# Optimization experiments

Measured on AMD Instinct MI355X. Metric: run time of the kernel, lower is better.

## Reference

```python
import jax, jax.numpy as jnp
import numpy as np

# ---- static geometry (matches init_kwargs) ----
B, S, D = 2, 4096, 2048
H, HD = 32, 64                      # num_heads, head_dim
HGRID, WGRID = 64, 64               # canvas h_dim, w_dim
TH, TW = 8, 16                      # tile size (th*tw = 128)
KH, KW = 16, 32                     # window (kernel) size
NTH, NTW = HGRID // TH, WGRID // TW
T = NTH * NTW                       # 32 tiles
TN = TH * TW                        # 128 tokens per tile
KTH, KTW = KH // TH, KW // TW
K = KTH * KTW                       # 4 kv tiles per query tile
SCALE = 1.0 / np.sqrt(HD)


def _kv_tile_ids():
    # For each query tile, the K kv tiles inside its (clamped) sliding window.
    qt = np.arange(T)
    qh, qw = qt // NTW, qt % NTW
    lbh, rbh = KTH // 2, KTH // 2 + (KTH % 2 - 1)
    lbw, rbw = KTW // 2, KTW // 2 + (KTW % 2 - 1)
    ch = np.clip(qh, lbh, NTH - 1 - rbh)
    cw = np.clip(qw, lbw, NTW - 1 - rbw)
    hh = ch[:, None] - lbh + np.arange(KTH)          # [T, KTH]
    ww = cw[:, None] - lbw + np.arange(KTW)          # [T, KTW]
    return (hh[:, :, None] * NTW + ww[:, None, :]).reshape(T, K)

KV_TILES = jnp.asarray(_kv_tile_ids())  # [T, K] int


def _to_tiles(x):
    # [B, S, H, HD] (row-major h,w) -> [B, H, T, TN, HD] (tile-major)
    x = x.reshape(B, NTH, TH, NTW, TW, H, HD)
    x = x.transpose(0, 5, 1, 3, 2, 4, 6)  # B,H,nth,ntw,th,tw,hd
    return x.reshape(B, H, T, TN, HD)


def _from_tiles(x):
    # [B, H, T, TN, HD] -> [B, S, H*HD]
    x = x.reshape(B, H, NTH, NTW, TH, TW, HD)
    x = x.transpose(0, 2, 4, 3, 5, 1, 6)  # B,nth,th,ntw,tw,H,hd
    return x.reshape(B, S, H * HD)


def setup_inputs() -> dict:
    key = jax.random.key(0)
    ks = jax.random.split(key, 5)
    sw = 1.0 / np.sqrt(D)
    return {
        "hidden_states": jax.random.normal(ks[0], (B, S, D), jnp.float32),
        "Wq": jax.random.normal(ks[1], (D, D), jnp.float32) * sw,
        "Wk": jax.random.normal(ks[2], (D, D), jnp.float32) * sw,
        "Wv": jax.random.normal(ks[3], (D, D), jnp.float32) * sw,
        "Wo": jax.random.normal(ks[4], (D, D), jnp.float32) * sw,
    }


def reference(hidden_states, Wq, Wk, Wv, Wo):
    # projections (weights stored [in, out]; equivalent to nn.Linear math)
    q = _to_tiles((hidden_states @ Wq).reshape(B, S, H, HD))  # [B,H,T,TN,HD]
    k = _to_tiles((hidden_states @ Wk).reshape(B, S, H, HD))
    v = _to_tiles((hidden_states @ Wv).reshape(B, S, H, HD))

    # gather the K allowed kv tiles for every query tile (block-sparse pattern)
    kg = k[:, :, KV_TILES].reshape(B, H, T, K * TN, HD)  # [B,H,T,K*TN,HD]
    vg = v[:, :, KV_TILES].reshape(B, H, T, K * TN, HD)

    # dense attention within each block (all gathered tokens are valid)
    scores = jnp.einsum("bhtqd,bhtkd->bhtqk", q, kg) * SCALE
    attn = jax.nn.softmax(scores, axis=-1)
    o = jnp.einsum("bhtqk,bhtkd->bhtqd", attn, vg)  # [B,H,T,TN,HD]

    return _from_tiles(o) @ Wo  # [B, S, D]
```

## Files before the change

### kernel.cpp

```cpp
#include <hip/hip_runtime.h>

typedef __bf16 bf16;
typedef __attribute__((ext_vector_type(8))) __bf16 bf16x8;
typedef __attribute__((ext_vector_type(4))) __bf16 bf16x4;
typedef __attribute__((ext_vector_type(4))) float f32x4;

#define MFMA16(a, b, c) __builtin_amdgcn_mfma_f32_16x16x32_bf16((a), (b), (c), 0, 0, 0)

__device__ __forceinline__ void gload16(const void* g, void* lds) {
  __builtin_amdgcn_global_load_lds(
      (__attribute__((address_space(1))) unsigned int*)(unsigned long long)g,
      (__attribute__((address_space(3))) unsigned int*)lds, 16, 0, 0);
}

__global__ void __launch_bounds__(256) cast_x_kernel(const float* __restrict__ X,
                                                     bf16* __restrict__ Xb) {
  int i = (blockIdx.x * 256 + threadIdx.x) * 4;
  f32x4 v = *(const f32x4*)(X + i);
  bf16x4 o;
  o[0] = (bf16)v[0]; o[1] = (bf16)v[1]; o[2] = (bf16)v[2]; o[3] = (bf16)v[3];
  *(bf16x4*)(Xb + i) = o;
}

__global__ void __launch_bounds__(256) transpose_w3_kernel(const float* __restrict__ Wq,
                                                           const float* __restrict__ Wk,
                                                           const float* __restrict__ Wv,
                                                           bf16* __restrict__ T0,
                                                           bf16* __restrict__ T1,
                                                           bf16* __restrict__ T2) {
  __shared__ float tile[64][65];
  int which = blockIdx.x >> 10;
  int bid = blockIdx.x & 1023;
  const float* W = which == 0 ? Wq : (which == 1 ? Wk : Wv);
  bf16* WT = which == 0 ? T0 : (which == 1 ? T1 : T2);
  int n0 = (bid & 31) * 64;
  int k0 = (bid >> 5) * 64;
  int tid = threadIdx.x;
  int r = tid >> 4;
  int c4 = (tid & 15) * 4;
#pragma unroll
  for (int i = 0; i < 4; ++i) {
    f32x4 v = *(const f32x4*)(W + (size_t)(k0 + r + i * 16) * 2048 + n0 + c4);
    tile[r + i * 16][c4 + 0] = v[0];
    tile[r + i * 16][c4 + 1] = v[1];
    tile[r + i * 16][c4 + 2] = v[2];
    tile[r + i * 16][c4 + 3] = v[3];
  }
  __syncthreads();
#pragma unroll
  for (int i = 0; i < 4; ++i) {
    int n = r + i * 16;
    bf16x4 o;
    o[0] = (bf16)tile[c4 + 0][n];
    o[1] = (bf16)tile[c4 + 1][n];
    o[2] = (bf16)tile[c4 + 2][n];
    o[3] = (bf16)tile[c4 + 3][n];
    *(bf16x4*)(WT + (size_t)(n0 + n) * 2048 + k0 + c4) = o;
  }
}

__global__ void __launch_bounds__(256) transpose_w_kernel(const float* __restrict__ W,
                                                          bf16* __restrict__ WT) {
  __shared__ float tile[64][65];
  int n0 = (blockIdx.x & 31) * 64;
  int k0 = (blockIdx.x >> 5) * 64;
  int tid = threadIdx.x;
  int r = tid >> 4;
  int c4 = (tid & 15) * 4;
#pragma unroll
  for (int i = 0; i < 4; ++i) {
    f32x4 v = *(const f32x4*)(W + (size_t)(k0 + r + i * 16) * 2048 + n0 + c4);
    tile[r + i * 16][c4 + 0] = v[0];
    tile[r + i * 16][c4 + 1] = v[1];
    tile[r + i * 16][c4 + 2] = v[2];
    tile[r + i * 16][c4 + 3] = v[3];
  }
  __syncthreads();
#pragma unroll
  for (int i = 0; i < 4; ++i) {
    int n = r + i * 16;
    bf16x4 o;
    o[0] = (bf16)tile[c4 + 0][n];
    o[1] = (bf16)tile[c4 + 1][n];
    o[2] = (bf16)tile[c4 + 2][n];
    o[3] = (bf16)tile[c4 + 3][n];
    *(bf16x4*)(WT + (size_t)(n0 + n) * 2048 + k0 + c4) = o;
  }
}

__device__ __forceinline__ void gemm256_core(const bf16* __restrict__ Ag,
                                             const bf16* __restrict__ Bg,
                                             char* lds, f32x4 (&acc)[8][4]) {
  const int tid = threadIdx.x;
  const int lane = tid & 63, wid = tid >> 6;
  const int g = lane >> 4, r16 = lane & 15;
  const int wm = wid >> 2, wn = wid & 3;
  const int swz = ((g ^ ((r16 >> 1) & 3)) << 4);

  const int srow = wid * 32 + (lane >> 2);
  const int scol = ((lane & 3) ^ ((lane >> 3) & 3)) * 8;
  const bf16* gA = Ag + (size_t)srow * 2048 + scol;
  const bf16* gB = Bg + (size_t)srow * 2048 + scol;
  char* sA = lds + wid * 2048;
  char* sB = lds + 16384 + wid * 2048;

  const int arow0 = wm * 128 + r16;
  const int brow0 = wn * 64 + r16;

#define STAGE_A(bf_, tt_)                              \
  {                                                    \
    char* d_ = sA + (bf_) * 32768;                     \
    const bf16* s_ = gA + (size_t)(tt_) * 32;          \
    gload16(s_, d_);                                   \
    gload16(s_ + (size_t)16 * 2048, d_ + 1024);        \
  }
#define STAGE_B(bf_, tt_)                              \
  {                                                    \
    char* d_ = sB + (bf_) * 32768;                     \
    const bf16* s_ = gB + (size_t)(tt_) * 32;          \
    gload16(s_, d_);                                   \
    gload16(s_ + (size_t)16 * 2048, d_ + 1024);        \
  }

  STAGE_A(0, 0) STAGE_B(0, 0) STAGE_A(1, 1) STAGE_B(1, 1)
  asm volatile("s_waitcnt vmcnt(4)" ::: "memory");
  __builtin_amdgcn_s_barrier();
  __builtin_amdgcn_sched_barrier(0);

  int c = 0;
  for (int t = 0; t < 64; ++t) {
    const char* Ab = lds + c * 32768;
    const char* Bb = Ab + 16384;
    int sbuf = c + 2; if (sbuf >= 3) sbuf -= 3;

    bf16x8 bfr[4], af[8];
#pragma unroll
    for (int j = 0; j < 4; ++j)
      bfr[j] = *(const bf16x8*)(Bb + (brow0 + j * 16) * 64 + swz);
#pragma unroll
    for (int i = 0; i < 8; ++i)
      af[i] = *(const bf16x8*)(Ab + (arow0 + i * 16) * 64 + swz);

    if (t < 62) { STAGE_A(sbuf, t + 2) STAGE_B(sbuf, t + 2) }

#pragma unroll
    for (int i = 0; i < 8; ++i)
#pragma unroll
      for (int j = 0; j < 4; ++j)
        acc[i][j] = MFMA16(af[i], bfr[j], acc[i][j]);

    if (t < 62) {
      asm volatile("s_waitcnt vmcnt(4)" ::: "memory");
    } else if (t == 62) {
      asm volatile("s_waitcnt vmcnt(0)" ::: "memory");
    }
    __builtin_amdgcn_s_barrier();
    __builtin_amdgcn_sched_barrier(0);

    c += 1; if (c >= 3) c -= 3;
  }
#undef STAGE_A
#undef STAGE_B
}

__global__ void __launch_bounds__(512, 2) gemm_qkv_kernel(
    const bf16* __restrict__ Xb, const bf16* __restrict__ W0, const bf16* __restrict__ W1,
    const bf16* __restrict__ W2, bf16* __restrict__ q_t, bf16* __restrict__ k_t,
    bf16* __restrict__ v_t) {
  __shared__ char lds[98304];
  int bid = blockIdx.x;
  int xcd = bid & 7, idx = bid >> 3;
  int by = xcd * 4 + idx / 24, bx = idx % 24;
  int which = bx >> 3;
  int m0 = by * 256, n0 = (bx & 7) * 256;
  const bf16* W = which == 0 ? W0 : (which == 1 ? W1 : W2);

  f32x4 acc[8][4] = {};
  gemm256_core(Xb + (size_t)m0 * 2048, W + (size_t)n0 * 2048, lds, acc);

  int lane = threadIdx.x & 63, wid = threadIdx.x >> 6;
  int g = lane >> 4, r16 = lane & 15;
  int wm = wid >> 2, wn = wid & 3;
#pragma unroll
  for (int i = 0; i < 8; ++i) {
#pragma unroll
    for (int r = 0; r < 4; ++r) {
      int m = m0 + wm * 128 + i * 16 + g * 4 + r;
      int b = m >> 12, s = m & 4095;
      int hg = s >> 6, wg = s & 63;
      int t = ((hg >> 3) << 2) + (wg >> 4);
      int tn = ((hg & 7) << 4) + (wg & 15);
#pragma unroll
      for (int j = 0; j < 4; ++j) {
        int n = n0 + wn * 64 + j * 16 + r16;
        int h = n >> 6, hd = n & 63;
        float val = acc[i][j][r];
        size_t base = ((size_t)(b * 32 + h) * 32 + t);
        if (which == 0)
          q_t[(base * 128 + tn) * 64 + hd] = (bf16)(val * 0.18033688056680255f);
        else if (which == 1)
          k_t[(base * 128 + tn) * 64 + hd] = (bf16)val;
        else
          v_t[(base * 64 + hd) * 128 + tn] = (bf16)val;
      }
    }
  }
}

__global__ void __launch_bounds__(512, 2) gemm_out_kernel(const bf16* __restrict__ A,
                                                          const bf16* __restrict__ W,
                                                          float* __restrict__ C) {
  __shared__ char lds[98304];
  int bid = blockIdx.x;
  int xcd = bid & 7, idx = bid >> 3;
  int by = xcd * 4 + idx / 8, bx = idx & 7;
  int m0 = by * 256, n0 = bx * 256;

  f32x4 acc[8][4] = {};
  gemm256_core(A + (size_t)m0 * 2048, W + (size_t)n0 * 2048, lds, acc);

  int lane = threadIdx.x & 63, wid = threadIdx.x >> 6;
  int g = lane >> 4, r16 = lane & 15;
  int wm = wid >> 2, wn = wid & 3;
#pragma unroll
  for (int i = 0; i < 8; ++i)
#pragma unroll
    for (int j = 0; j < 4; ++j)
#pragma unroll
      for (int r = 0; r < 4; ++r) {
        int m = m0 + wm * 128 + i * 16 + g * 4 + r;
        int n = n0 + wn * 64 + j * 16 + r16;
        C[(size_t)m * 2048 + n] = acc[i][j][r];
      }
}

__global__ void __launch_bounds__(256) attn_kernel(const bf16* __restrict__ q_t,
                                                   const bf16* __restrict__ k_t,
                                                   const bf16* __restrict__ v_t,
                                                   bf16* __restrict__ o_bf) {
  __shared__ char Pl[128 * 256];
  int bid = blockIdx.x;
  int bh = (bid & 7) * 8 + (bid >> 8);
  int t = (bid >> 3) & 31;
  int h = bh & 31, b = bh >> 5;
  int tid = threadIdx.x, w = tid >> 6, lane = tid & 63;
  int g = lane >> 4, r16 = lane & 15;

  const size_t qoff = ((size_t)bh * 32 + t) * (128 * 64);
  bf16x8 qf[2][2];
#pragma unroll
  for (int mf = 0; mf < 2; ++mf)
#pragma unroll
    for (int kf = 0; kf < 2; ++kf)
      qf[mf][kf] = *(const bf16x8*)&q_t[qoff + (size_t)(w * 32 + mf * 16 + r16) * 64 + kf * 32 + g * 8];

  bf16x8 ones;
#pragma unroll
  for (int j = 0; j < 8; ++j) ones[j] = (bf16)1.0f;

  f32x4 oacc[2][4] = {};
  f32x4 lacc[2] = {};

  int qh = t >> 2, qw = t & 3;
  int ch = qh < 1 ? 1 : (qh > 7 ? 7 : qh);
  int cw = qw < 1 ? 1 : (qw > 3 ? 3 : qw);

  for (int c = 0; c < 4; ++c) {
    int vt = (ch - 1 + (c >> 1)) * 4 + (cw - 1 + (c & 1));
    const bf16* Kt = k_t + ((size_t)bh * 32 + vt) * (128 * 64);
    const bf16* Vt = v_t + ((size_t)bh * 32 + vt) * (128 * 64);

    f32x4 s[2][8];
#pragma unroll
    for (int nf = 0; nf < 8; ++nf) {
      bf16x8 kf0 = *(const bf16x8*)&Kt[(nf * 16 + r16) * 64 + g * 8];
      bf16x8 kf1 = *(const bf16x8*)&Kt[(nf * 16 + r16) * 64 + 32 + g * 8];
#pragma unroll
      for (int mf = 0; mf < 2; ++mf) {
        f32x4 z = {};
        z = MFMA16(qf[mf][0], kf0, z);
        z = MFMA16(qf[mf][1], kf1, z);
        s[mf][nf] = z;
      }
    }

#pragma unroll
    for (int mf = 0; mf < 2; ++mf)
#pragma unroll
      for (int r = 0; r < 4; ++r) {
        int row = w * 32 + mf * 16 + g * 4 + r;
        int rb = row * 256;
        int swzp = (row & 7) << 4;
#pragma unroll
        for (int nf = 0; nf < 8; ++nf) {
          int addr = (rb + (nf * 16 + r16) * 2) ^ swzp;
          *(bf16*)(Pl + addr) = (bf16)__builtin_amdgcn_exp2f(s[mf][nf][r]);
        }
      }
    __syncthreads();

#pragma unroll
    for (int ks = 0; ks < 4; ++ks) {
      bf16x8 pf[2];
#pragma unroll
      for (int mf = 0; mf < 2; ++mf) {
        int row = w * 32 + mf * 16 + r16;
        int addr = (row * 256 + ks * 64 + g * 16) ^ ((row & 7) << 4);
        pf[mf] = *(const bf16x8*)(Pl + addr);
      }
      bf16x8 vf[4];
#pragma unroll
      for (int hf = 0; hf < 4; ++hf)
        vf[hf] = *(const bf16x8*)&Vt[(hf * 16 + r16) * 128 + ks * 32 + g * 8];
#pragma unroll
      for (int mf = 0; mf < 2; ++mf) {
        lacc[mf] = MFMA16(pf[mf], ones, lacc[mf]);
#pragma unroll
        for (int hf = 0; hf < 4; ++hf)
          oacc[mf][hf] = MFMA16(pf[mf], vf[hf], oacc[mf][hf]);
      }
    }
    __syncthreads();
  }

  int nth = t >> 2, ntw = t & 3;
#pragma unroll
  for (int mf = 0; mf < 2; ++mf)
#pragma unroll
    for (int r = 0; r < 4; ++r) {
      float inv = __builtin_amdgcn_rcpf(lacc[mf][r]);
      int tn = w * 32 + mf * 16 + g * 4 + r;
      int stok = (nth * 8 + (tn >> 4)) * 64 + ntw * 16 + (tn & 15);
#pragma unroll
      for (int hf = 0; hf < 4; ++hf) {
        int col = h * 64 + hf * 16 + r16;
        o_bf[((size_t)b * 4096 + stok) * 2048 + col] = (bf16)(oacc[mf][hf][r] * inv);
      }
    }
}

extern "C" void kernel_launch(void* const* d_in, const int* in_sizes, int n_in,
                              void* d_out, int out_size, void* d_ws, size_t ws_size,
                              hipStream_t stream) {
  const float* X = (const float*)d_in[0];
  const float* Wq = (const float*)d_in[1];
  const float* Wk = (const float*)d_in[2];
  const float* Wv = (const float*)d_in[3];
  const float* Wo = (const float*)d_in[4];
  float* out = (float*)d_out;
  char* ws = (char*)d_ws;
  if (ws_size < 159383552u) return;

  bf16* Xb  = (bf16*)(ws + 0);
  bf16* WT0 = (bf16*)(ws + 33554432u);
  bf16* WT1 = (bf16*)(ws + 41943040u);
  bf16* WT2 = (bf16*)(ws + 50331648u);
  bf16* q_t = (bf16*)(ws + 58720256u);
  bf16* k_t = (bf16*)(ws + 92274688u);
  bf16* v_t = (bf16*)(ws + 125829120u);
  bf16* o_bf = Xb;

  cast_x_kernel<<<16384, 256, 0, stream>>>(X, Xb);
  transpose_w3_kernel<<<3072, 256, 0, stream>>>(Wq, Wk, Wv, WT0, WT1, WT2);
  gemm_qkv_kernel<<<768, 512, 0, stream>>>(Xb, WT0, WT1, WT2, q_t, k_t, v_t);
  attn_kernel<<<2048, 256, 0, stream>>>(q_t, k_t, v_t, o_bf);
  transpose_w_kernel<<<1024, 256, 0, stream>>>(Wo, WT0);
  gemm_out_kernel<<<256, 512, 0, stream>>>(o_bf, WT0, out);
}
```

Measured before the change: 458.0 us.

## Deepen GEMM LDS pipeline to four stages with register double-buffered fragments

The shared 256x256 GEMM core moves from a 3-buffer LDS ring to a 4-buffer ring, with loads issued three tiles ahead. The loop is unrolled by two with ping-pong register fragment sets, so the LDS reads for the next k-step are issued before the MFMAs of the current step. The aim is to hide global-load and LDS-read latency behind matrix math. In exchange, LDS per block grows to 128 KB, which likely allows only one block per CU despite the launch bound of two. The second fragment set also raises register pressure.

Measured after the change: 455.9 us. About the same (-0.5%).

```diff
diff --git a/kernel.cpp b/kernel.cpp
--- a/kernel.cpp
+++ b/kernel.cpp
@@ -107,67 +107,73 @@
   const int arow0 = wm * 128 + r16;
   const int brow0 = wn * 64 + r16;
 
-#define STAGE_A(bf_, tt_)                              \
-  {                                                    \
-    char* d_ = sA + (bf_) * 32768;                     \
-    const bf16* s_ = gA + (size_t)(tt_) * 32;          \
-    gload16(s_, d_);                                   \
-    gload16(s_ + (size_t)16 * 2048, d_ + 1024);        \
-  }
-#define STAGE_B(bf_, tt_)                              \
-  {                                                    \
-    char* d_ = sB + (bf_) * 32768;                     \
-    const bf16* s_ = gB + (size_t)(tt_) * 32;          \
-    gload16(s_, d_);                                   \
-    gload16(s_ + (size_t)16 * 2048, d_ + 1024);        \
-  }
-
-  STAGE_A(0, 0) STAGE_B(0, 0) STAGE_A(1, 1) STAGE_B(1, 1)
+#define STAGE(bf_, tt_)                                                  \
+  {                                                                      \
+    char* dA_ = sA + (bf_) * 32768;                                      \
+    const bf16* sA_ = gA + (size_t)(tt_) * 32;                           \
+    gload16(sA_, dA_);                                                   \
+    gload16(sA_ + (size_t)16 * 2048, dA_ + 1024);                        \
+    char* dB_ = sB + (bf_) * 32768;                                      \
+    const bf16* sB_ = gB + (size_t)(tt_) * 32;                           \
+    gload16(sB_, dB_);                                                   \
+    gload16(sB_ + (size_t)16 * 2048, dB_ + 1024);                        \
+  }
+
+#define READF(fa_, fb_, base_)                                           \
+  {                                                                      \
+    const char* Ab_ = lds + (base_);                                     \
+    const char* Bb_ = Ab_ + 16384;                                       \
+    _Pragma("unroll") for (int j_ = 0; j_ < 4; ++j_)                     \
+      fb_[j_] = *(const bf16x8*)(Bb_ + (brow0 + j_ * 16) * 64 + swz);    \
+    _Pragma("unroll") for (int i_ = 0; i_ < 8; ++i_)                     \
+      fa_[i_] = *(const bf16x8*)(Ab_ + (arow0 + i_ * 16) * 64 + swz);    \
+  }
+
+#define MF(fa_, fb_)                                                     \
+  {                                                                      \
+    _Pragma("unroll") for (int i_ = 0; i_ < 8; ++i_)                     \
+    _Pragma("unroll") for (int j_ = 0; j_ < 4; ++j_)                     \
+      acc[i_][j_] = MFMA16(fa_[i_], fb_[j_], acc[i_][j_]);               \
+  }
+
+#define VMCHAIN(u_)                                                      \
+  if ((u_) <= 60)      { asm volatile("s_waitcnt vmcnt(4)" ::: "memory"); } \
+  else if ((u_) == 61) { asm volatile("s_waitcnt vmcnt(0)" ::: "memory"); }
+
+  bf16x8 fA0[8], fB0[4], fA1[8], fB1[4];
+
+  STAGE(0, 0) STAGE(1, 1) STAGE(2, 2)
   asm volatile("s_waitcnt vmcnt(4)" ::: "memory");
   __builtin_amdgcn_s_barrier();
-  __builtin_amdgcn_sched_barrier(0);
-
-  int c = 0;
-  for (int t = 0; t < 64; ++t) {
-    const char* Ab = lds + c * 32768;
-    const char* Bb = Ab + 16384;
-    int sbuf = c + 2; if (sbuf >= 3) sbuf -= 3;
-
-    bf16x8 bfr[4], af[8];
-#pragma unroll
-    for (int j = 0; j < 4; ++j)
-      bfr[j] = *(const bf16x8*)(Bb + (brow0 + j * 16) * 64 + swz);
-#pragma unroll
-    for (int i = 0; i < 8; ++i)
-      af[i] = *(const bf16x8*)(Ab + (arow0 + i * 16) * 64 + swz);
-
-    if (t < 62) { STAGE_A(sbuf, t + 2) STAGE_B(sbuf, t + 2) }
-
-#pragma unroll
-    for (int i = 0; i < 8; ++i)
-#pragma unroll
-      for (int j = 0; j < 4; ++j)
-        acc[i][j] = MFMA16(af[i], bfr[j], acc[i][j]);
-
-    if (t < 62) {
-      asm volatile("s_waitcnt vmcnt(4)" ::: "memory");
-    } else if (t == 62) {
-      asm volatile("s_waitcnt vmcnt(0)" ::: "memory");
-    }
+  READF(fA0, fB0, 0)
+
+  for (int t = 0; t < 64; t += 2) {
+    if (t + 3 < 64) STAGE((t + 3) & 3, t + 3)
+    VMCHAIN(t)
+    READF(fA1, fB1, (size_t)((t + 1) & 3) * 32768)
+    __builtin_amdgcn_sched_barrier(0);
+    MF(fA0, fB0)
     __builtin_amdgcn_s_barrier();
     __builtin_amdgcn_sched_barrier(0);
-
-    c += 1; if (c >= 3) c -= 3;
-  }
-#undef STAGE_A
-#undef STAGE_B
+    if (t + 4 < 64) STAGE((t + 4) & 3, t + 4)
+    VMCHAIN(t + 1)
+    READF(fA0, fB0, (size_t)((t + 2) & 3) * 32768)
+    __builtin_amdgcn_sched_barrier(0);
+    MF(fA1, fB1)
+    __builtin_amdgcn_s_barrier();
+    __builtin_amdgcn_sched_barrier(0);
+  }
+#undef STAGE
+#undef READF
+#undef MF
+#undef VMCHAIN
 }
 
 __global__ void __launch_bounds__(512, 2) gemm_qkv_kernel(
     const bf16* __restrict__ Xb, const bf16* __restrict__ W0, const bf16* __restrict__ W1,
     const bf16* __restrict__ W2, bf16* __restrict__ q_t, bf16* __restrict__ k_t,
     bf16* __restrict__ v_t) {
-  __shared__ char lds[98304];
+  __shared__ char lds[131072];
   int bid = blockIdx.x;
   int xcd = bid & 7, idx = bid >> 3;
   int by = xcd * 4 + idx / 24, bx = idx % 24;
@@ -210,7 +216,7 @@
 __global__ void __launch_bounds__(512, 2) gemm_out_kernel(const bf16* __restrict__ A,
                                                           const bf16* __restrict__ W,
                                                           float* __restrict__ C) {
-  __shared__ char lds[98304];
+  __shared__ char lds[131072];
   int bid = blockIdx.x;
   int xcd = bid & 7, idx = bid >> 3;
   int by = xcd * 4 + idx / 8, bx = idx & 7;
```

## Restructure GEMM mainloop into double-buffered K=64 tiles with interleaved quarter-stage loads

Applied to the files above, without the earlier changes.

Replaces the triple-buffered K=32 pipeline in the shared GEMM core with a double-buffered K=64 scheme. Each iteration is split into four quarters that interleave global-to-LDS staging of the next tile with MFMA blocks over half the A rows, and s_setprio raises wave priority around the MFMA bursts. The aim is to halve loop trips and barrier overhead per K step and to overlap memory with compute more finely. LDS per block grows from 96KB to 128KB, which may limit occupancy against the launch bound of two blocks per CU, and more barriers are issued per iteration.

Measured after the change: 460.6 us. About the same (+0.6%).

```diff
diff --git a/kernel.cpp b/kernel.cpp
--- a/kernel.cpp
+++ b/kernel.cpp
@@ -97,77 +97,87 @@
   const int wm = wid >> 2, wn = wid & 3;
   const int swz = ((g ^ ((r16 >> 1) & 3)) << 4);
 
-  const int srow = wid * 32 + (lane >> 2);
-  const int scol = ((lane & 3) ^ ((lane >> 3) & 3)) * 8;
-  const bf16* gA = Ag + (size_t)srow * 2048 + scol;
-  const bf16* gB = Bg + (size_t)srow * 2048 + scol;
-  char* sA = lds + wid * 2048;
-  char* sB = lds + 16384 + wid * 2048;
+  const int srow = wid * 16 + (lane >> 2);
+  const int sg = ((lane & 3) ^ ((lane >> 3) & 3)) * 8;
+  const bf16* gA = Ag + (size_t)srow * 2048 + sg;
+  const bf16* gB = Bg + (size_t)srow * 2048 + sg;
+  const int sdst = wid * 1024;
 
   const int arow0 = wm * 128 + r16;
   const int brow0 = wn * 64 + r16;
 
-#define STAGE_A(bf_, tt_)                              \
-  {                                                    \
-    char* d_ = sA + (bf_) * 32768;                     \
-    const bf16* s_ = gA + (size_t)(tt_) * 32;          \
-    gload16(s_, d_);                                   \
-    gload16(s_ + (size_t)16 * 2048, d_ + 1024);        \
-  }
-#define STAGE_B(bf_, tt_)                              \
-  {                                                    \
-    char* d_ = sB + (bf_) * 32768;                     \
-    const bf16* s_ = gB + (size_t)(tt_) * 32;          \
-    gload16(s_, d_);                                   \
-    gload16(s_ + (size_t)16 * 2048, d_ + 1024);        \
-  }
-
-  STAGE_A(0, 0) STAGE_B(0, 0) STAGE_A(1, 1) STAGE_B(1, 1)
-  asm volatile("s_waitcnt vmcnt(4)" ::: "memory");
+#define STAGEU(ab_, kk_, buf_, tt_)                                       \
+  {                                                                       \
+    const bf16* s_ = ((ab_) ? gB : gA) + (size_t)(tt_) * 64 + (kk_) * 32; \
+    char* d_ = lds + (buf_) + (ab_) * 32768 + (kk_) * 16384 + sdst;       \
+    gload16(s_, d_);                                                      \
+    gload16(s_ + (size_t)128 * 2048, d_ + 8192);                          \
+  }
+
+#define RD_B(kk_, buf_)                                                   \
+  {                                                                       \
+    const char* Bb_ = lds + (buf_) + 32768 + (kk_) * 16384;               \
+    _Pragma("unroll") for (int j_ = 0; j_ < 4; ++j_)                      \
+      bfr[j_] = *(const bf16x8*)(Bb_ + (brow0 + j_ * 16) * 64 + swz);     \
+  }
+
+#define RD_A(kk_, buf_, i0_)                                              \
+  {                                                                       \
+    const char* Ab_ = lds + (buf_) + (kk_) * 16384;                       \
+    _Pragma("unroll") for (int i_ = 0; i_ < 4; ++i_)                      \
+      afr[i_] = *(const bf16x8*)(Ab_ + (arow0 + ((i0_) + i_) * 16) * 64 + swz); \
+  }
+
+#define MFQ(i0_)                                                          \
+  __builtin_amdgcn_s_barrier();                                           \
+  asm volatile("s_waitcnt lgkmcnt(0)" ::: "memory");                      \
+  __builtin_amdgcn_sched_barrier(0);                                      \
+  __builtin_amdgcn_s_setprio(1);                                          \
+  _Pragma("unroll") for (int i_ = 0; i_ < 4; ++i_)                        \
+  _Pragma("unroll") for (int j_ = 0; j_ < 4; ++j_)                        \
+    acc[(i0_) + i_][j_] = MFMA16(afr[i_], bfr[j_], acc[(i0_) + i_][j_]);  \
+  __builtin_amdgcn_s_setprio(0);
+
+  bf16x8 afr[4], bfr[4];
+
+  STAGEU(0, 0, 0, 0) STAGEU(1, 0, 0, 0) STAGEU(0, 1, 0, 0) STAGEU(1, 1, 0, 0)
+  asm volatile("s_waitcnt vmcnt(0)" ::: "memory");
   __builtin_amdgcn_s_barrier();
-  __builtin_amdgcn_sched_barrier(0);
-
-  int c = 0;
-  for (int t = 0; t < 64; ++t) {
-    const char* Ab = lds + c * 32768;
-    const char* Bb = Ab + 16384;
-    int sbuf = c + 2; if (sbuf >= 3) sbuf -= 3;
-
-    bf16x8 bfr[4], af[8];
-#pragma unroll
-    for (int j = 0; j < 4; ++j)
-      bfr[j] = *(const bf16x8*)(Bb + (brow0 + j * 16) * 64 + swz);
-#pragma unroll
-    for (int i = 0; i < 8; ++i)
-      af[i] = *(const bf16x8*)(Ab + (arow0 + i * 16) * 64 + swz);
-
-    if (t < 62) { STAGE_A(sbuf, t + 2) STAGE_B(sbuf, t + 2) }
-
-#pragma unroll
-    for (int i = 0; i < 8; ++i)
-#pragma unroll
-      for (int j = 0; j < 4; ++j)
-        acc[i][j] = MFMA16(af[i], bfr[j], acc[i][j]);
-
-    if (t < 62) {
-      asm volatile("s_waitcnt vmcnt(4)" ::: "memory");
-    } else if (t == 62) {
-      asm volatile("s_waitcnt vmcnt(0)" ::: "memory");
-    }
+
+  for (int T = 0; T < 32; ++T) {
+    const int buf = (T & 1) << 16;
+    const int nbf = buf ^ 65536;
+    RD_B(0, buf) RD_A(0, buf, 0)
+    if (T < 31) STAGEU(0, 0, nbf, T + 1)
+    MFQ(0)
     __builtin_amdgcn_s_barrier();
-    __builtin_amdgcn_sched_barrier(0);
-
-    c += 1; if (c >= 3) c -= 3;
-  }
-#undef STAGE_A
-#undef STAGE_B
+    RD_A(0, buf, 4)
+    if (T < 31) STAGEU(1, 0, nbf, T + 1)
+    MFQ(4)
+    if (T < 31) { asm volatile("s_waitcnt vmcnt(4)" ::: "memory"); }
+    else        { asm volatile("s_waitcnt vmcnt(0)" ::: "memory"); }
+    __builtin_amdgcn_s_barrier();
+    RD_B(1, buf) RD_A(1, buf, 0)
+    if (T < 31) STAGEU(0, 1, nbf, T + 1)
+    MFQ(0)
+    __builtin_amdgcn_s_barrier();
+    RD_A(1, buf, 4)
+    if (T < 31) STAGEU(1, 1, nbf, T + 1)
+    MFQ(4)
+    if (T < 31) { asm volatile("s_waitcnt vmcnt(4)" ::: "memory"); }
+    __builtin_amdgcn_s_barrier();
+  }
+#undef STAGEU
+#undef RD_B
+#undef RD_A
+#undef MFQ
 }
 
 __global__ void __launch_bounds__(512, 2) gemm_qkv_kernel(
     const bf16* __restrict__ Xb, const bf16* __restrict__ W0, const bf16* __restrict__ W1,
     const bf16* __restrict__ W2, bf16* __restrict__ q_t, bf16* __restrict__ k_t,
     bf16* __restrict__ v_t) {
-  __shared__ char lds[98304];
+  __shared__ char lds[131072];
   int bid = blockIdx.x;
   int xcd = bid & 7, idx = bid >> 3;
   int by = xcd * 4 + idx / 24, bx = idx % 24;
@@ -210,7 +220,7 @@
 __global__ void __launch_bounds__(512, 2) gemm_out_kernel(const bf16* __restrict__ A,
                                                           const bf16* __restrict__ W,
                                                           float* __restrict__ C) {
-  __shared__ char lds[98304];
+  __shared__ char lds[131072];
   int bid = blockIdx.x;
   int xcd = bid & 7, idx = bid >> 3;
   int by = xcd * 4 + idx / 8, bx = idx & 7;
```
